# Optimization experiments

Measured on AMD Instinct MI355X. Metric: run time of the kernel, lower is better.

## Reference

```python
import jax, jax.numpy as jnp
import numpy as np

EPS = 1e-7        # min norm to avoid div-by-zero
BALL_EPS = 1e-5   # Poincare-ball boundary clip


def _norm(x):
    return jnp.maximum(jnp.linalg.norm(x, axis=-1, keepdims=True), EPS)


def expmap0(u, c):
    sc = jnp.sqrt(c)
    n = _norm(u)
    return jnp.tanh(sc * n) * u / (sc * n)


def logmap0(p, c):
    sc = jnp.sqrt(c)
    n = _norm(p)
    return jnp.arctanh(jnp.minimum(sc * n, 1.0 - BALL_EPS)) * p / (sc * n)


def proj(x, c):
    # project onto the ball of radius (1-eps)/sqrt(c)
    n = _norm(x)
    maxn = (1.0 - BALL_EPS) / jnp.sqrt(c)
    return jnp.where(n > maxn, x * (maxn / n), x)


def mobius_matvec(W, x, c):
    # Mobius matrix-vector multiply on the Poincare ball
    sc = jnp.sqrt(c)
    xn = _norm(x)                       # [N,1]
    mx = x @ W                          # [N,D]
    mxn = _norm(mx)
    t = jnp.tanh((mxn / xn) * jnp.arctanh(jnp.minimum(sc * xn, 1.0 - BALL_EPS)))
    return t * mx / (sc * mxn)


def spmm(rows, cols, vals, x):
    # sparse(adj) @ x, adjacency in COO form
    return jax.ops.segment_sum(vals[:, None] * x[cols], rows, num_segments=x.shape[0])


def hgc_layer(x, rows, cols, vals, W, c, c_lin):
    t = logmap0(x, c)                               # to tangent space at origin
    h = proj(mobius_matvec(W, t, c_lin), c_lin)     # LinearHyperbolic (c=1.0, no activation)
    s = spmm(rows, cols, vals, h)                   # HyperbolicAggregation: adj @ h
    agg = proj(expmap0(s, c), c)
    a = jax.nn.relu(logmap0(agg, c))                # ActivationHyperbolic (relu, c_in=c_out=c)
    return proj(expmap0(a, c), c)


def setup_inputs() -> dict:
    key = jax.random.key(0)
    ks = jax.random.split(key, 7)
    N, D, E = 10000, 1433, 100000
    x = jax.random.normal(ks[0], (N, D), jnp.float32) * 0.1  # keep points off the boundary
    rows = jax.random.randint(ks[1], (E,), 0, N)
    cols = jax.random.randint(ks[2], (E,), 0, N)
    vals = jax.random.uniform(ks[3], (E,), jnp.float32) / 10.0  # ~normalized adjacency weights
    scale = 1.0 / np.sqrt(D)
    W0 = jax.random.normal(ks[4], (D, D), jnp.float32) * scale
    W1 = jax.random.normal(ks[5], (D, D), jnp.float32) * scale
    W2 = jax.random.normal(ks[6], (D, D), jnp.float32) * scale
    return {"x": x, "W0": W0, "W1": W1, "W2": W2, "vals": vals, "rows": rows, "cols": cols}


def reference(x, W0, W1, W2, vals, rows, cols):
    c = jnp.float32(0.4)       # c_map == c0 for every layer in the source
    c_lin = jnp.float32(1.0)   # LinearHyperbolic hard-coded c
    h = expmap0(x, c)
    for W in (W0, W1, W2):
        h = hgc_layer(h, rows, cols, vals, W, c, c_lin)
    return h
```

## Files before the change

### kernel.cpp

```cpp
#include <hip/hip_runtime.h>

typedef unsigned short u16;
typedef unsigned int   u32;

#define M_ROWS 10000
#define D_DIM  1433
#define KPAD   1536
#define MPAD   10240
#define N_EDGE 100000
#define HPAD   1440
#define HP32   720
#define NKT    24
#define EPS    1e-7f
#define BEPS   1e-5f
#define SC     0.6324555320336759f

typedef __bf16 bf16x8 __attribute__((ext_vector_type(8)));
typedef float  f32x4  __attribute__((ext_vector_type(4)));
typedef u32    u32x4  __attribute__((ext_vector_type(4)));

__device__ __forceinline__ u16 f2bf(float f) {
  union { float f; unsigned u; } v; v.f = f;
  unsigned r = v.u + 0x7FFFu + ((v.u >> 16) & 1u);
  return (u16)(r >> 16);
}
__device__ __forceinline__ u32 pack2bf(float lo, float hi) {
  return (u32)f2bf(lo) | ((u32)f2bf(hi) << 16);
}
__device__ __forceinline__ float bflo(u32 u) { return __uint_as_float(u << 16); }
__device__ __forceinline__ float bfhi(u32 u) { return __uint_as_float(u & 0xFFFF0000u); }

__device__ __forceinline__ float atanh_f(float y) {
  return 0.5f * logf((1.f + y) / (1.f - y));
}

__device__ __forceinline__ void gl_lds16(const u16* g, u16* l) {
  __builtin_amdgcn_global_load_lds((const __attribute__((address_space(1))) void*)(const void*)g,
                                   (__attribute__((address_space(3))) void*)(void*)l,
                                   16, 0, 0);
}

__global__ __launch_bounds__(256, 3) void gemm128(
    const u16* __restrict__ A,
    const u16* __restrict__ B,
    u16* __restrict__ C,
    float* __restrict__ nrm)
{
  __shared__ u16 ldsA[128 * 64];
  __shared__ u16 ldsB[128 * 64];

  const int tid  = threadIdx.x;
  const int lane = tid & 63;
  const int w    = tid >> 6;
  const int wr   = w >> 1;
  const int wc   = w & 1;

  const int flat = blockIdx.x;
  const int wgid = (flat & 7) * 120 + (flat >> 3);
  const int gy = wgid % 12;
  const int gx = wgid / 12;
  const long arow0 = (long)gx * 128;
  const long brow0 = (long)gy * 128;

  f32x4 acc[4][4] = {};

  const int sr8 = lane >> 3;
  const int scb = ((lane & 7) << 4) ^ (sr8 << 4);

  auto STAGE = [&](int kt) {
    const long k0 = (long)kt * 64 + (scb >> 1);
#pragma unroll
    for (int l = 0; l < 4; ++l) {
      const int r   = l * 32 + w * 8 + sr8;
      const int dst = l * 2048 + w * 512;
      gl_lds16(A + (arow0 + r) * KPAD + k0, &ldsA[dst]);
      gl_lds16(B + (brow0 + r) * KPAD + k0, &ldsB[dst]);
    }
  };

  for (int kt = 0; kt < NKT; ++kt) {
    STAGE(kt);
    __syncthreads();
#pragma unroll
    for (int ks = 0; ks < 2; ++ks) {
      bf16x8 af[4], bfr[4];
#pragma unroll
      for (int mi = 0; mi < 4; ++mi) {
        const int row = wr * 64 + mi * 16 + (lane & 15);
        const int kb  = (ks * 64 + ((lane >> 4) << 4)) ^ ((row & 7) << 4);
        af[mi] = *(const bf16x8*)&ldsA[row * 64 + (kb >> 1)];
      }
#pragma unroll
      for (int ni = 0; ni < 4; ++ni) {
        const int row = wc * 64 + ni * 16 + (lane & 15);
        const int kb  = (ks * 64 + ((lane >> 4) << 4)) ^ ((row & 7) << 4);
        bfr[ni] = *(const bf16x8*)&ldsB[row * 64 + (kb >> 1)];
      }
#pragma unroll
      for (int mi = 0; mi < 4; ++mi)
#pragma unroll
        for (int ni = 0; ni < 4; ++ni)
          acc[mi][ni] = __builtin_amdgcn_mfma_f32_16x16x32_bf16(af[mi], bfr[ni], acc[mi][ni], 0, 0, 0);
    }
    __syncthreads();
  }

  const int orw = (lane >> 4) * 4;
  const int ocl = lane & 15;

#pragma unroll
  for (int mi = 0; mi < 4; ++mi)
#pragma unroll
    for (int r = 0; r < 4; ++r) {
      float s = 0.f;
#pragma unroll
      for (int ni = 0; ni < 4; ++ni) {
        const long j = brow0 + wc * 64 + ni * 16 + ocl;
        const float v = acc[mi][ni][r];
        s += (j < D_DIM) ? v * v : 0.f;
      }
      s += __shfl_xor(s, 1, 64);
      s += __shfl_xor(s, 2, 64);
      s += __shfl_xor(s, 4, 64);
      s += __shfl_xor(s, 8, 64);
      if ((lane & 15) == 0)
        atomicAdd(&nrm[arow0 + wr * 64 + mi * 16 + orw + r], s);
    }

#pragma unroll
  for (int mi = 0; mi < 4; ++mi) {
    const long i0 = arow0 + wr * 64 + mi * 16 + orw;
    if (i0 >= M_ROWS) continue;
#pragma unroll
    for (int ni = 0; ni < 4; ++ni) {
      const long j = brow0 + wc * 64 + ni * 16 + ocl;
      if (j >= HPAD) continue;
#pragma unroll
      for (int r = 0; r < 4; ++r) {
        const long i = i0 + r;
        if (i < M_ROWS) C[i * HPAD + j] = (j < D_DIM) ? f2bf(acc[mi][ni][r]) : (u16)0;
      }
    }
  }
}

__device__ __forceinline__ float2 block_reduce2(float a, float b) {
  __shared__ float sa[4], sb[4];
#pragma unroll
  for (int off = 32; off > 0; off >>= 1) {
    a += __shfl_down(a, off, 64);
    b += __shfl_down(b, off, 64);
  }
  const int tid = threadIdx.x;
  if ((tid & 63) == 0) { sa[tid >> 6] = a; sb[tid >> 6] = b; }
  __syncthreads();
  const float ra = sa[0] + sa[1] + sa[2] + sa[3];
  const float rb = sb[0] + sb[1] + sb[2] + sb[3];
  __syncthreads();
  return make_float2(ra, rb);
}

__global__ __launch_bounds__(256) void pre_k(const float* __restrict__ x,
                                             u16* __restrict__ t,
                                             float* __restrict__ xn) {
  const long i = blockIdx.x;
  const int tid = threadIdx.x;
  u16* trow = t + i * KPAD;
  if (i >= M_ROWS) {
#pragma unroll
    for (int jj = 0; jj < 6; ++jj) { int j = tid + jj * 256; if (j < KPAD) trow[j] = 0; }
    return;
  }
  const float* xr = x + i * D_DIM;
  float v[6]; float s2 = 0.f;
#pragma unroll
  for (int jj = 0; jj < 6; ++jj) {
    int j = tid + jj * 256;
    v[jj] = (j < D_DIM) ? xr[j] : 0.f;
    s2 += v[jj] * v[jj];
  }
  s2 = block_reduce2(s2, 0.f).x;
  const float nx_t = sqrtf(s2);
  const float nx   = fmaxf(nx_t, EPS);
  const float al   = tanhf(SC * nx) / (SC * nx);
  const float n1   = fmaxf(al * nx_t, EPS);
  const float be   = atanh_f(fminf(SC * n1, 1.f - BEPS)) / (SC * n1);
  const float sca  = al * be;
  if (tid == 0) xn[i] = fmaxf(sca * nx_t, EPS);
#pragma unroll
  for (int jj = 0; jj < 6; ++jj) {
    int j = tid + jj * 256;
    if (j < KPAD) trow[j] = (j < D_DIM) ? f2bf(sca * v[jj]) : (u16)0;
  }
}

__global__ void zero_f(float* p, int n) {
  int i = blockIdx.x * 256 + threadIdx.x;
  if (i < n) p[i] = 0.f;
}

__global__ void fold_k(const int* __restrict__ ecol, const float* __restrict__ eval,
                       const float* __restrict__ nrm, const float* __restrict__ xn,
                       u32* __restrict__ pe, int E) {
  const int e = blockIdx.x * 256 + threadIdx.x;
  if (e >= E) return;
  const int c = ecol[e];
  const float realn = sqrtf(nrm[c]);
  const float mxn   = fmaxf(realn, EPS);
  const float xi    = xn[c];
  const float tf    = tanhf((mxn / xi) * atanh_f(fminf(xi, 1.f - BEPS)));
  float S = tf / mxn;
  const float hn = fmaxf(S * realn, EPS);
  const float maxn = 1.f - BEPS;
  if (hn > maxn) S *= maxn / hn;
  pe[e] = ((u32)c << 16) | (u32)f2bf(eval[e] * S);
}

__global__ __launch_bounds__(256) void spmm_post(const int* __restrict__ rp,
                                                 const u32* __restrict__ pe,
                                                 const u32* __restrict__ mxp,
                                                 u16* __restrict__ t,
                                                 float* __restrict__ xn,
                                                 float* __restrict__ out,
                                                 const int last) {
  const long r = blockIdx.x;
  const int tid = threadIdx.x;
  if (r >= M_ROWS) {
    if (!last && tid < 192) {
      u32* trow32 = (u32*)(t + r * KPAD);
#pragma unroll
      for (int k = 0; k < 4; ++k) trow32[4 * tid + k] = 0u;
    }
    return;
  }
  const bool act = tid < 180;
  const long boff = 4 * tid;
  float a[8] = {0.f, 0.f, 0.f, 0.f, 0.f, 0.f, 0.f, 0.f};
  const int e0 = rp[r], e1 = rp[r + 1];
  int e = e0;
  for (; e + 7 < e1; e += 8) {
    u32 pp[8];
#pragma unroll
    for (int j = 0; j < 8; ++j) pp[j] = pe[e + j];
    if (act) {
      u32x4 q[8];
#pragma unroll
      for (int j = 0; j < 8; ++j)
        q[j] = *(const u32x4*)&mxp[(long)(pp[j] >> 16) * HP32 + boff];
#pragma unroll
      for (int j = 0; j < 8; ++j) {
        const float w = bflo(pp[j]);
#pragma unroll
        for (int k = 0; k < 4; ++k) {
          a[2 * k]     += w * bflo(q[j][k]);
          a[2 * k + 1] += w * bfhi(q[j][k]);
        }
      }
    }
  }
  for (; e + 3 < e1; e += 4) {
    u32 pp[4];
#pragma unroll
    for (int j = 0; j < 4; ++j) pp[j] = pe[e + j];
    if (act) {
      u32x4 q[4];
#pragma unroll
      for (int j = 0; j < 4; ++j)
        q[j] = *(const u32x4*)&mxp[(long)(pp[j] >> 16) * HP32 + boff];
#pragma unroll
      for (int j = 0; j < 4; ++j) {
        const float w = bflo(pp[j]);
#pragma unroll
        for (int k = 0; k < 4; ++k) {
          a[2 * k]     += w * bflo(q[j][k]);
          a[2 * k + 1] += w * bfhi(q[j][k]);
        }
      }
    }
  }
  for (; e < e1; ++e) {
    const u32 p0 = pe[e];
    if (act) {
      const u32x4 q0 = *(const u32x4*)&mxp[(long)(p0 >> 16) * HP32 + boff];
      const float w0 = bflo(p0);
#pragma unroll
      for (int k = 0; k < 4; ++k) {
        a[2 * k]     += w0 * bflo(q0[k]);
        a[2 * k + 1] += w0 * bfhi(q0[k]);
      }
    }
  }
  float s2 = 0.f, s2p = 0.f;
#pragma unroll
  for (int k = 0; k < 8; ++k) {
    const int col = 8 * tid + k;
    const float v = (act && col < D_DIM) ? a[k] : 0.f;
    a[k] = v;
    s2 += v * v;
    const float p = fmaxf(v, 0.f);
    s2p += p * p;
  }
  const float2 red = block_reduce2(s2, s2p);
  const float ns_t  = sqrtf(red.x);
  const float nsp_t = sqrtf(red.y);
  const float maxn = (1.f - BEPS) / SC;
  const float ns = fmaxf(ns_t, EPS);
  const float al = tanhf(SC * ns) / (SC * ns);
  const float n1 = fmaxf(al * ns_t, EPS);
  const float be = (n1 > maxn) ? (maxn / n1) : 1.f;
  const float n2 = fmaxf(be * al * ns_t, EPS);
  const float lam = atanh_f(fminf(SC * n2, 1.f - BEPS)) / (SC * n2);
  const float g = lam * be * al;
  const float na_t = g * nsp_t;
  const float n3 = fmaxf(na_t, EPS);
  const float mu = tanhf(SC * n3) / (SC * n3);
  const float n4 = fmaxf(mu * na_t, EPS);
  const float nu = (n4 > maxn) ? (maxn / n4) : 1.f;
  const float T = nu * mu * g;
  if (last) {
    if (act) {
      float* orow = out + r * (long)D_DIM;
#pragma unroll
      for (int k = 0; k < 8; ++k) {
        const int col = 8 * tid + k;
        if (col < D_DIM) orow[col] = T * fmaxf(a[k], 0.f);
      }
    }
  } else {
    const float nh_t = T * nsp_t;
    const float n5 = fmaxf(nh_t, EPS);
    const float kap = atanh_f(fminf(SC * n5, 1.f - BEPS)) / (SC * n5);
    const float F = kap * T;
    if (tid == 0) xn[r] = fmaxf(F * nsp_t, EPS);
    u32* trow32 = (u32*)(t + r * KPAD);
    if (act) {
#pragma unroll
      for (int k = 0; k < 4; ++k)
        trow32[4 * tid + k] = pack2bf(F * fmaxf(a[2 * k], 0.f), F * fmaxf(a[2 * k + 1], 0.f));
    } else if (tid < 192) {
#pragma unroll
      for (int k = 0; k < 4; ++k) trow32[4 * tid + k] = 0u;
    }
  }
}

__global__ void wt_conv(const float* __restrict__ W, u16* __restrict__ Wt) {
  __shared__ float tile[32][33];
  const int kb = blockIdx.x * 32, nb = blockIdx.y * 32;
  const int tx = threadIdx.x, ty = threadIdx.y;
#pragma unroll
  for (int r = 0; r < 32; r += 8) {
    const int k = kb + ty + r, n = nb + tx;
    tile[ty + r][tx] = (k < D_DIM && n < D_DIM) ? W[(long)k * D_DIM + n] : 0.f;
  }
  __syncthreads();
#pragma unroll
  for (int r = 0; r < 32; r += 8) {
    const int n = nb + ty + r, k = kb + tx;
    if (n < KPAD && k < KPAD) Wt[(long)n * KPAD + k] = f2bf(tile[tx][ty + r]);
  }
}

__global__ void zero_int(int* p, int n) {
  int i = blockIdx.x * 256 + threadIdx.x;
  if (i < n) p[i] = 0;
}
__global__ void hist_k(const int* __restrict__ rows, int* __restrict__ counts, int E) {
  int e = blockIdx.x * 256 + threadIdx.x;
  if (e < E) atomicAdd(&counts[rows[e]], 1);
}
__global__ __launch_bounds__(1024) void scan_rp(const int* __restrict__ counts,
                                                int* __restrict__ rp, int n) {
  __shared__ int sd[1024];
  __shared__ int carry_s;
  const int tid = threadIdx.x;
  if (tid == 0) { carry_s = 0; rp[0] = 0; }
  __syncthreads();
  for (int base = 0; base < n; base += 1024) {
    const int i = base + tid;
    sd[tid] = (i < n) ? counts[i] : 0;
    __syncthreads();
    for (int off = 1; off < 1024; off <<= 1) {
      const int tv = (tid >= off) ? sd[tid - off] : 0;
      __syncthreads();
      sd[tid] += tv;
      __syncthreads();
    }
    const int carry = carry_s;
    if (i < n) rp[i + 1] = carry + sd[tid];
    __syncthreads();
    if (tid == 1023) carry_s = carry + sd[1023];
    __syncthreads();
  }
}
__global__ void scatter_k(const int* __restrict__ rows, const int* __restrict__ cols,
                          const float* __restrict__ vals, const int* __restrict__ rp,
                          int* __restrict__ cursor, int* __restrict__ ecol,
                          float* __restrict__ eval, int E) {
  int e = blockIdx.x * 256 + threadIdx.x;
  if (e < E) {
    const int r = rows[e];
    const int pos = rp[r] + atomicAdd(&cursor[r], 1);
    ecol[pos] = cols[e];
    eval[pos] = vals[e];
  }
}

extern "C" void kernel_launch(void* const* d_in, const int* in_sizes, int n_in,
                              void* d_out, int out_size, void* d_ws, size_t ws_size,
                              hipStream_t stream) {
  (void)in_sizes; (void)n_in; (void)out_size; (void)ws_size;
  const float* x    = (const float*)d_in[0];
  const float* W[3] = {(const float*)d_in[1], (const float*)d_in[2], (const float*)d_in[3]};
  const float* vals = (const float*)d_in[4];
  const int*   rows = (const int*)d_in[5];
  const int*   cols = (const int*)d_in[6];
  float* out = (float*)d_out;

  char* base = (char*)d_ws;
  size_t off = 0;
  auto take = [&](size_t bytes) {
    void* q = base + off;
    off = (off + bytes + 255) & ~(size_t)255;
    return q;
  };
  u16*   t    = (u16*)take((size_t)MPAD * KPAD * 2);
  u16*   Wt   = (u16*)take((size_t)KPAD * KPAD * 2);
  u16*   mx   = (u16*)take((size_t)M_ROWS * HPAD * 2);
  float* nrm3 = (float*)take((size_t)3 * MPAD * 4);
  float* xn   = (float*)take((size_t)M_ROWS * 4);
  int*   cnt  = (int*)take((size_t)M_ROWS * 2 * 4);
  int*   rp   = (int*)take((size_t)(M_ROWS + 1) * 4);
  int*   ecol = (int*)take((size_t)N_EDGE * 4);
  float* eval = (float*)take((size_t)N_EDGE * 4);
  u32*   pe   = (u32*)take((size_t)N_EDGE * 4);

  zero_int<<<(2 * M_ROWS + 255) / 256, 256, 0, stream>>>(cnt, 2 * M_ROWS);
  hist_k<<<(N_EDGE + 255) / 256, 256, 0, stream>>>(rows, cnt, N_EDGE);
  scan_rp<<<1, 1024, 0, stream>>>(cnt, rp, M_ROWS);
  scatter_k<<<(N_EDGE + 255) / 256, 256, 0, stream>>>(rows, cols, vals, rp,
                                                      cnt + M_ROWS, ecol, eval, N_EDGE);
  zero_f<<<(3 * MPAD + 255) / 256, 256, 0, stream>>>(nrm3, 3 * MPAD);

  pre_k<<<MPAD, 256, 0, stream>>>(x, t, xn);

  for (int L = 0; L < 3; ++L) {
    float* nrm = nrm3 + (size_t)L * MPAD;
    wt_conv<<<dim3(48, 48), dim3(32, 8), 0, stream>>>(W[L], Wt);
    gemm128<<<960, 256, 0, stream>>>(t, Wt, mx, nrm);
    fold_k<<<(N_EDGE + 255) / 256, 256, 0, stream>>>(ecol, eval, nrm, xn, pe, N_EDGE);
    spmm_post<<<MPAD, 256, 0, stream>>>(rp, pe, (const u32*)mx, t, xn, out, (L == 2) ? 1 : 0);
  }
}
```

Before: 383.5 us.

## Process one row per wavefront in spmm_post and pad GEMM output to 1536

Rewrites the SpMM/post kernel so each 64-lane wavefront handles a whole row, with every lane covering 24 columns in three 16-byte chunks. The block-level shared-memory reduction becomes a wave-level shuffle reduction, and there are four rows per block. The GEMM output row stride is widened to 1536 so the chunked loads line up and the bounds check on columns is dropped. This removes idle threads and block syncs. In exchange it uses more registers per thread, gives less memory-level parallelism per row, and makes the GEMM write extra padded columns.

```diff
diff --git a/kernel.cpp b/kernel.cpp
--- a/kernel.cpp
+++ b/kernel.cpp
@@ -8,8 +8,8 @@
 #define KPAD   1536
 #define MPAD   10240
 #define N_EDGE 100000
-#define HPAD   1440
-#define HP32   720
+#define HPAD   1536
+#define HP32   768
 #define NKT    24
 #define EPS    1e-7f
 #define BEPS   1e-5f
@@ -134,7 +134,6 @@
 #pragma unroll
     for (int ni = 0; ni < 4; ++ni) {
       const long j = brow0 + wc * 64 + ni * 16 + ocl;
-      if (j >= HPAD) continue;
 #pragma unroll
       for (int r = 0; r < 4; ++r) {
         const long i = i0 + r;
@@ -223,86 +222,80 @@
                                                  float* __restrict__ xn,
                                                  float* __restrict__ out,
                                                  const int last) {
-  const long r = blockIdx.x;
-  const int tid = threadIdx.x;
+  const int lane = threadIdx.x & 63;
+  const long r = (long)blockIdx.x * 4 + (threadIdx.x >> 6);
+  const int li4 = lane * 4;
   if (r >= M_ROWS) {
-    if (!last && tid < 192) {
+    if (!last && r < MPAD) {
       u32* trow32 = (u32*)(t + r * KPAD);
-#pragma unroll
-      for (int k = 0; k < 4; ++k) trow32[4 * tid + k] = 0u;
+      const u32x4 z = {0u, 0u, 0u, 0u};
+#pragma unroll
+      for (int c = 0; c < 3; ++c) *(u32x4*)&trow32[c * 256 + li4] = z;
     }
     return;
   }
-  const bool act = tid < 180;
-  const long boff = 4 * tid;
-  float a[8] = {0.f, 0.f, 0.f, 0.f, 0.f, 0.f, 0.f, 0.f};
+  float a[24] = {};
   const int e0 = rp[r], e1 = rp[r + 1];
   int e = e0;
-  for (; e + 7 < e1; e += 8) {
-    u32 pp[8];
-#pragma unroll
-    for (int j = 0; j < 8; ++j) pp[j] = pe[e + j];
-    if (act) {
-      u32x4 q[8];
-#pragma unroll
-      for (int j = 0; j < 8; ++j)
-        q[j] = *(const u32x4*)&mxp[(long)(pp[j] >> 16) * HP32 + boff];
-#pragma unroll
-      for (int j = 0; j < 8; ++j) {
-        const float w = bflo(pp[j]);
-#pragma unroll
-        for (int k = 0; k < 4; ++k) {
-          a[2 * k]     += w * bflo(q[j][k]);
-          a[2 * k + 1] += w * bfhi(q[j][k]);
-        }
-      }
-    }
-  }
   for (; e + 3 < e1; e += 4) {
     u32 pp[4];
 #pragma unroll
     for (int j = 0; j < 4; ++j) pp[j] = pe[e + j];
-    if (act) {
-      u32x4 q[4];
-#pragma unroll
-      for (int j = 0; j < 4; ++j)
-        q[j] = *(const u32x4*)&mxp[(long)(pp[j] >> 16) * HP32 + boff];
-#pragma unroll
-      for (int j = 0; j < 4; ++j) {
-        const float w = bflo(pp[j]);
+    u32x4 q[4][3];
+#pragma unroll
+    for (int j = 0; j < 4; ++j) {
+      const u32* src = &mxp[(long)(pp[j] >> 16) * HP32];
+#pragma unroll
+      for (int c = 0; c < 3; ++c) q[j][c] = *(const u32x4*)&src[c * 256 + li4];
+    }
+#pragma unroll
+    for (int j = 0; j < 4; ++j) {
+      const float w = bflo(pp[j]);
+#pragma unroll
+      for (int c = 0; c < 3; ++c)
 #pragma unroll
         for (int k = 0; k < 4; ++k) {
-          a[2 * k]     += w * bflo(q[j][k]);
-          a[2 * k + 1] += w * bfhi(q[j][k]);
+          a[c * 8 + 2 * k]     += w * bflo(q[j][c][k]);
+          a[c * 8 + 2 * k + 1] += w * bfhi(q[j][c][k]);
         }
-      }
     }
   }
   for (; e < e1; ++e) {
     const u32 p0 = pe[e];
-    if (act) {
-      const u32x4 q0 = *(const u32x4*)&mxp[(long)(p0 >> 16) * HP32 + boff];
-      const float w0 = bflo(p0);
+    const u32* src = &mxp[(long)(p0 >> 16) * HP32];
+    const float w0 = bflo(p0);
+#pragma unroll
+    for (int c = 0; c < 3; ++c) {
+      const u32x4 q0 = *(const u32x4*)&src[c * 256 + li4];
 #pragma unroll
       for (int k = 0; k < 4; ++k) {
-        a[2 * k]     += w0 * bflo(q0[k]);
-        a[2 * k + 1] += w0 * bfhi(q0[k]);
+        a[c * 8 + 2 * k]     += w0 * bflo(q0[k]);
+        a[c * 8 + 2 * k + 1] += w0 * bfhi(q0[k]);
       }
     }
   }
   float s2 = 0.f, s2p = 0.f;
 #pragma unroll
-  for (int k = 0; k < 8; ++k) {
-    const int col = 8 * tid + k;
-    const float v = (act && col < D_DIM) ? a[k] : 0.f;
-    a[k] = v;
-    s2 += v * v;
-    const float p = fmaxf(v, 0.f);
-    s2p += p * p;
-  }
-  const float2 red = block_reduce2(s2, s2p);
-  const float ns_t  = sqrtf(red.x);
-  const float nsp_t = sqrtf(red.y);
+  for (int c = 0; c < 3; ++c)
+#pragma unroll
+    for (int k = 0; k < 4; ++k)
+#pragma unroll
+      for (int h = 0; h < 2; ++h) {
+        const int col = (c * 256 + li4 + k) * 2 + h;
+        const int idx = c * 8 + 2 * k + h;
+        const float v = (col < D_DIM) ? a[idx] : 0.f;
+        a[idx] = v;
+        s2 += v * v;
+        const float p = fmaxf(v, 0.f);
+        s2p += p * p;
+      }
+#pragma unroll
+  for (int off = 32; off > 0; off >>= 1) {
+    s2  += __shfl_xor(s2, off, 64);
+    s2p += __shfl_xor(s2p, off, 64);
+  }
+  const float ns_t  = sqrtf(s2);
+  const float nsp_t = sqrtf(s2p);
   const float maxn = (1.f - BEPS) / SC;
   const float ns = fmaxf(ns_t, EPS);
   const float al = tanhf(SC * ns) / (SC * ns);
@@ -318,28 +311,31 @@
   const float nu = (n4 > maxn) ? (maxn / n4) : 1.f;
   const float T = nu * mu * g;
   if (last) {
-    if (act) {
-      float* orow = out + r * (long)D_DIM;
-#pragma unroll
-      for (int k = 0; k < 8; ++k) {
-        const int col = 8 * tid + k;
-        if (col < D_DIM) orow[col] = T * fmaxf(a[k], 0.f);
-      }
-    }
+    float* orow = out + r * (long)D_DIM;
+#pragma unroll
+    for (int c = 0; c < 3; ++c)
+#pragma unroll
+      for (int k = 0; k < 4; ++k)
+#pragma unroll
+        for (int h = 0; h < 2; ++h) {
+          const int col = (c * 256 + li4 + k) * 2 + h;
+          if (col < D_DIM) orow[col] = T * fmaxf(a[c * 8 + 2 * k + h], 0.f);
+        }
   } else {
     const float nh_t = T * nsp_t;
     const float n5 = fmaxf(nh_t, EPS);
     const float kap = atanh_f(fminf(SC * n5, 1.f - BEPS)) / (SC * n5);
     const float F = kap * T;
-    if (tid == 0) xn[r] = fmaxf(F * nsp_t, EPS);
+    if (lane == 0) xn[r] = fmaxf(F * nsp_t, EPS);
     u32* trow32 = (u32*)(t + r * KPAD);
-    if (act) {
+#pragma unroll
+    for (int c = 0; c < 3; ++c) {
+      u32x4 wv;
 #pragma unroll
       for (int k = 0; k < 4; ++k)
-        trow32[4 * tid + k] = pack2bf(F * fmaxf(a[2 * k], 0.f), F * fmaxf(a[2 * k + 1], 0.f));
-    } else if (tid < 192) {
-#pragma unroll
-      for (int k = 0; k < 4; ++k) trow32[4 * tid + k] = 0u;
+        wv[k] = pack2bf(F * fmaxf(a[c * 8 + 2 * k], 0.f),
+                        F * fmaxf(a[c * 8 + 2 * k + 1], 0.f));
+      *(u32x4*)&trow32[c * 256 + li4] = wv;
     }
   }
 }
@@ -449,6 +445,6 @@
     wt_conv<<<dim3(48, 48), dim3(32, 8), 0, stream>>>(W[L], Wt);
     gemm128<<<960, 256, 0, stream>>>(t, Wt, mx, nrm);
     fold_k<<<(N_EDGE + 255) / 256, 256, 0, stream>>>(ecol, eval, nrm, xn, pe, N_EDGE);
-    spmm_post<<<MPAD, 256, 0, stream>>>(rp, pe, (const u32*)mx, t, xn, out, (L == 2) ? 1 : 0);
-  }
-}
+    spmm_post<<<MPAD / 4, 256, 0, stream>>>(rp, pe, (const u32*)mx, t, xn, out, (L == 2) ? 1 : 0);
+  }
+}
```

Result: no change. 385.2 us (+0.4%).
